# Optimization experiments

Measured on AMD Instinct MI355X. Metric: run time of the kernel, lower is better.

The kernel has to match this reference:

```python
import jax, jax.numpy as jnp
import numpy as np

B, IN_F, OUT_F = 1024, 256, 256
GRID_SIZE, K = 5, 3  # grid_size, spline_order
N_BASIS = GRID_SIZE + K


def _make_grid():
    h = (1.0 - (-1.0)) / GRID_SIZE
    return jnp.linspace(-1.0 - K * h, 1.0 + K * h, GRID_SIZE + 2 * K + 1, dtype=jnp.float32)


def compute_bspline_basis(x, grid, k):
    # x: (N,), grid: (G + 2k + 1,) -> (N, G + k)
    x = x[:, None]
    bases = ((x >= grid[:-1]) & (x < grid[1:])).astype(x.dtype)
    for p in range(1, k + 1):
        n = bases.shape[1] - 1
        left_den = jnp.clip(grid[p:p + n] - grid[:n], 1e-8)
        left = (x - grid[:n]) / left_den * bases[:, :n]
        right_den = jnp.clip(grid[p + 1:p + 1 + n] - grid[1:1 + n], 1e-8)
        right = (grid[p + 1:p + 1 + n] - x) / right_den * bases[:, 1:1 + n]
        bases = left + right
    # boundary fix: x at/above last interior knot falls into last basis
    bases = bases.at[:, -1].add((x[:, 0] >= grid[-k - 1]).astype(x.dtype))
    return bases


def setup_inputs() -> dict:
    key = jax.random.key(0)
    kx, kc, kb = jax.random.split(key, 3)
    x = jax.random.normal(kx, (B, IN_F), dtype=jnp.float32)
    coeff = jax.random.normal(kc, (OUT_F, IN_F, N_BASIS), dtype=jnp.float32) / np.sqrt(IN_F * N_BASIS)
    base_weight = jax.random.normal(kb, (OUT_F, IN_F), dtype=jnp.float32) / np.sqrt(IN_F)
    spline_weight = jnp.ones((OUT_F, IN_F), dtype=jnp.float32)
    grid = _make_grid()
    return {"x": x, "grid": grid, "coeff": coeff,
            "base_weight": base_weight, "spline_weight": spline_weight}


def reference(x, grid, coeff, base_weight, spline_weight):
    batch = x.shape[0]
    bases = compute_bspline_basis(x.reshape(-1), grid, K)          # (B*in, n_basis)
    bases = bases.reshape(batch, IN_F, N_BASIS)                     # (b, i, n)
    spline_out = jnp.einsum('bin,oin->boi', bases, coeff)           # (b, o, i)
    spline_out = spline_out * spline_weight[None, :, :]
    base_out = jax.nn.silu(x)[:, None, :] * base_weight[None, :, :]  # (b, o, i)
    return (spline_out + base_out).sum(axis=2)                      # (b, o)
```

## Files before the change

### kernel.cpp

```cpp
#include <hip/hip_runtime.h>
#include <hip/hip_bf16.h>

#define B_SZ   1024
#define IN_F   256
#define OUT_F  256
#define NB     9
#define KTOT   (IN_F * NB)
#define NGRID  12

typedef __attribute__((ext_vector_type(8))) short  bf16x8;
typedef __attribute__((ext_vector_type(16))) float f32x16;

__global__ __launch_bounds__(256) void kan_prep(
    const float* __restrict__ x,
    const float* __restrict__ grid,
    const float* __restrict__ coeff,
    const float* __restrict__ bw,
    const float* __restrict__ sw,
    __hip_bfloat16* __restrict__ phi,
    __hip_bfloat16* __restrict__ W) {
  if (blockIdx.x < (B_SZ * IN_F) / 256) {
    int idx = blockIdx.x * 256 + threadIdx.x;
    float g[NGRID];
#pragma unroll
    for (int j = 0; j < NGRID; ++j) g[j] = grid[j];
    float xv = x[idx];

    float bas[NGRID - 1];
#pragma unroll
    for (int j = 0; j < NGRID - 1; ++j)
      bas[j] = (xv >= g[j] && xv < g[j + 1]) ? 1.0f : 0.0f;

#pragma unroll
    for (int p = 1; p <= 3; ++p) {
      int n = NGRID - 1 - p;
#pragma unroll
      for (int j = 0; j < n; ++j) {
        float ld = g[p + j] - g[j];
        if (ld < 1e-8f) ld = 1e-8f;
        float rd = g[p + 1 + j] - g[j + 1];
        if (rd < 1e-8f) rd = 1e-8f;
        bas[j] = (xv - g[j]) * __builtin_amdgcn_rcpf(ld) * bas[j] +
                 (g[p + 1 + j] - xv) * __builtin_amdgcn_rcpf(rd) * bas[j + 1];
      }
    }
    bas[7] += (xv >= g[NGRID - 4]) ? 1.0f : 0.0f;
    float sil = xv / (1.0f + __expf(-xv));

    int b = idx >> 8;
    int i = idx & 255;
    __hip_bfloat16* dst = phi + b * KTOT + i;
#pragma unroll
    for (int n = 0; n < 8; ++n) dst[n * IN_F] = __float2bfloat16(bas[n]);
    dst[8 * IN_F] = __float2bfloat16(sil);
  } else {
    int idx = (blockIdx.x - (B_SZ * IN_F) / 256) * 256 + threadIdx.x;
    int o = idx >> 8;
    int i = idx & 255;
    float s = sw[idx];
    const float* c = coeff + (size_t)idx * 8;
    __hip_bfloat16* dst = W + o * KTOT + i;
#pragma unroll
    for (int n = 0; n < 8; ++n)
      dst[n * IN_F] = __float2bfloat16(s * c[n]);
    dst[8 * IN_F] = __float2bfloat16(bw[idx]);
  }
}

#define KSEG (KTOT / 8)

__global__ __launch_bounds__(512) void kan_gemm(
    const __hip_bfloat16* __restrict__ phi,
    const __hip_bfloat16* __restrict__ W,
    float* __restrict__ out) {
  __shared__ float partial[8][32 * 32];

  int tid  = threadIdx.x;
  int wave = tid >> 6;
  int lane = tid & 63;
  int bm = (blockIdx.x & 31) * 32;
  int bn = (blockIdx.x >> 5) * 32;
  int r = lane & 31;
  int h = lane >> 5;

  const short* ap = (const short*)(phi + (size_t)(bm + r) * KTOT) + wave * KSEG + h * 8;
  const short* bp = (const short*)(W   + (size_t)(bn + r) * KTOT) + wave * KSEG + h * 8;

  f32x16 acc;
#pragma unroll
  for (int g = 0; g < 16; ++g) acc[g] = 0.0f;

#pragma unroll 6
  for (int k = 0; k < KSEG; k += 16) {
    bf16x8 a = *(const bf16x8*)(ap + k);
    bf16x8 b = *(const bf16x8*)(bp + k);
    acc = __builtin_amdgcn_mfma_f32_32x32x16_bf16(a, b, acc, 0, 0, 0);
  }

  float* pw = &partial[wave][0];
#pragma unroll
  for (int g = 0; g < 16; ++g) {
    int row = (g & 3) + 8 * (g >> 2) + 4 * h;
    pw[row * 32 + r] = acc[g];
  }
  __syncthreads();

  int e0 = tid * 2;
  float s0 = 0.0f, s1 = 0.0f;
#pragma unroll
  for (int w = 0; w < 8; ++w) {
    s0 += partial[w][e0];
    s1 += partial[w][e0 + 1];
  }
  int row = e0 >> 5, col = e0 & 31;
  float2 v = make_float2(s0, s1);
  *(float2*)&out[(size_t)(bm + row) * OUT_F + bn + col] = v;
}

extern "C" void kernel_launch(void* const* d_in, const int* in_sizes, int n_in,
                              void* d_out, int out_size, void* d_ws, size_t ws_size,
                              hipStream_t stream) {
  const float* x     = (const float*)d_in[0];
  const float* grid  = (const float*)d_in[1];
  const float* coeff = (const float*)d_in[2];
  const float* bw    = (const float*)d_in[3];
  const float* sw    = (const float*)d_in[4];
  float* out = (float*)d_out;

  __hip_bfloat16* phi = (__hip_bfloat16*)d_ws;
  __hip_bfloat16* W   = phi + (size_t)B_SZ * KTOT;

  kan_prep<<<(B_SZ * IN_F + OUT_F * IN_F) / 256, 256, 0, stream>>>(
      x, grid, coeff, bw, sw, phi, W);
  kan_gemm<<<(B_SZ / 32) * (OUT_F / 32), 512, 0, stream>>>(phi, W, out);
}
```

Before: 76.75 us.

## Fuse prep and GEMM into one cooperative kernel with grid sync

Merges the basis/weight preparation kernel and the MFMA GEMM kernel into a single cooperative launch of 256 blocks of 512 threads. Each thread computes two activation rows' worth of basis values and possibly one weight entry, then a grid-wide barrier separates the prep and GEMM phases. This removes one kernel launch and the gap between them. The cost is a grid sync and a cooperative launch with fewer threads doing the prep work.

```diff
diff --git a/kernel.cpp b/kernel.cpp
--- a/kernel.cpp
+++ b/kernel.cpp
@@ -1,5 +1,8 @@
 #include <hip/hip_runtime.h>
 #include <hip/hip_bf16.h>
+#include <hip/hip_cooperative_groups.h>
+
+namespace cg = cooperative_groups;
 
 #define B_SZ   1024
 #define IN_F   256
@@ -7,73 +10,79 @@
 #define NB     9
 #define KTOT   (IN_F * NB)
 #define NGRID  12
+#define NTHR   (256 * 512)
 
 typedef __attribute__((ext_vector_type(8))) short  bf16x8;
 typedef __attribute__((ext_vector_type(16))) float f32x16;
 
-__global__ __launch_bounds__(256) void kan_prep(
+#define KSEG (KTOT / 8)
+
+__global__ __launch_bounds__(512) void kan_fused(
     const float* __restrict__ x,
     const float* __restrict__ grid,
     const float* __restrict__ coeff,
     const float* __restrict__ bw,
     const float* __restrict__ sw,
     __hip_bfloat16* __restrict__ phi,
-    __hip_bfloat16* __restrict__ W) {
-  if (blockIdx.x < (B_SZ * IN_F) / 256) {
-    int idx = blockIdx.x * 256 + threadIdx.x;
+    __hip_bfloat16* __restrict__ W,
+    float* __restrict__ out) {
+  __shared__ float partial[8][32 * 32];
+
+  int t = blockIdx.x * 512 + threadIdx.x;
+
+  {
     float g[NGRID];
 #pragma unroll
     for (int j = 0; j < NGRID; ++j) g[j] = grid[j];
-    float xv = x[idx];
-
-    float bas[NGRID - 1];
-#pragma unroll
-    for (int j = 0; j < NGRID - 1; ++j)
-      bas[j] = (xv >= g[j] && xv < g[j + 1]) ? 1.0f : 0.0f;
 
 #pragma unroll
-    for (int p = 1; p <= 3; ++p) {
-      int n = NGRID - 1 - p;
+    for (int rep = 0; rep < 2; ++rep) {
+      int idx = t + rep * NTHR;
+      float xv = x[idx];
+
+      float bas[NGRID - 1];
 #pragma unroll
-      for (int j = 0; j < n; ++j) {
-        float ld = g[p + j] - g[j];
-        if (ld < 1e-8f) ld = 1e-8f;
-        float rd = g[p + 1 + j] - g[j + 1];
-        if (rd < 1e-8f) rd = 1e-8f;
-        bas[j] = (xv - g[j]) * __builtin_amdgcn_rcpf(ld) * bas[j] +
-                 (g[p + 1 + j] - xv) * __builtin_amdgcn_rcpf(rd) * bas[j + 1];
+      for (int j = 0; j < NGRID - 1; ++j)
+        bas[j] = (xv >= g[j] && xv < g[j + 1]) ? 1.0f : 0.0f;
+
+#pragma unroll
+      for (int p = 1; p <= 3; ++p) {
+        int n = NGRID - 1 - p;
+#pragma unroll
+        for (int j = 0; j < n; ++j) {
+          float ld = g[p + j] - g[j];
+          if (ld < 1e-8f) ld = 1e-8f;
+          float rd = g[p + 1 + j] - g[j + 1];
+          if (rd < 1e-8f) rd = 1e-8f;
+          bas[j] = (xv - g[j]) * __builtin_amdgcn_rcpf(ld) * bas[j] +
+                   (g[p + 1 + j] - xv) * __builtin_amdgcn_rcpf(rd) * bas[j + 1];
+        }
       }
+      bas[7] += (xv >= g[NGRID - 4]) ? 1.0f : 0.0f;
+      float sil = xv / (1.0f + __expf(-xv));
+
+      int b = idx >> 8;
+      int i = idx & 255;
+      __hip_bfloat16* dst = phi + b * KTOT + i;
+#pragma unroll
+      for (int n = 0; n < 8; ++n) dst[n * IN_F] = __float2bfloat16(bas[n]);
+      dst[8 * IN_F] = __float2bfloat16(sil);
     }
-    bas[7] += (xv >= g[NGRID - 4]) ? 1.0f : 0.0f;
-    float sil = xv / (1.0f + __expf(-xv));
+  }
 
-    int b = idx >> 8;
-    int i = idx & 255;
-    __hip_bfloat16* dst = phi + b * KTOT + i;
-#pragma unroll
-    for (int n = 0; n < 8; ++n) dst[n * IN_F] = __float2bfloat16(bas[n]);
-    dst[8 * IN_F] = __float2bfloat16(sil);
-  } else {
-    int idx = (blockIdx.x - (B_SZ * IN_F) / 256) * 256 + threadIdx.x;
-    int o = idx >> 8;
-    int i = idx & 255;
-    float s = sw[idx];
-    const float* c = coeff + (size_t)idx * 8;
+  if (t < OUT_F * IN_F) {
+    int o = t >> 8;
+    int i = t & 255;
+    float s = sw[t];
+    const float* c = coeff + (size_t)t * 8;
     __hip_bfloat16* dst = W + o * KTOT + i;
 #pragma unroll
     for (int n = 0; n < 8; ++n)
       dst[n * IN_F] = __float2bfloat16(s * c[n]);
-    dst[8 * IN_F] = __float2bfloat16(bw[idx]);
+    dst[8 * IN_F] = __float2bfloat16(bw[t]);
   }
-}
 
-#define KSEG (KTOT / 8)
-
-__global__ __launch_bounds__(512) void kan_gemm(
-    const __hip_bfloat16* __restrict__ phi,
-    const __hip_bfloat16* __restrict__ W,
-    float* __restrict__ out) {
-  __shared__ float partial[8][32 * 32];
+  cg::this_grid().sync();
 
   int tid  = threadIdx.x;
   int wave = tid >> 6;
@@ -88,7 +97,7 @@
 
   f32x16 acc;
 #pragma unroll
-  for (int g = 0; g < 16; ++g) acc[g] = 0.0f;
+  for (int gg = 0; gg < 16; ++gg) acc[gg] = 0.0f;
 
 #pragma unroll 6
   for (int k = 0; k < KSEG; k += 16) {
@@ -99,9 +108,9 @@
 
   float* pw = &partial[wave][0];
 #pragma unroll
-  for (int g = 0; g < 16; ++g) {
-    int row = (g & 3) + 8 * (g >> 2) + 4 * h;
-    pw[row * 32 + r] = acc[g];
+  for (int gg = 0; gg < 16; ++gg) {
+    int row = (gg & 3) + 8 * (gg >> 2) + 4 * h;
+    pw[row * 32 + r] = acc[gg];
   }
   __syncthreads();
 
@@ -130,7 +139,7 @@
   __hip_bfloat16* phi = (__hip_bfloat16*)d_ws;
   __hip_bfloat16* W   = phi + (size_t)B_SZ * KTOT;
 
-  kan_prep<<<(B_SZ * IN_F + OUT_F * IN_F) / 256, 256, 0, stream>>>(
-      x, grid, coeff, bw, sw, phi, W);
-  kan_gemm<<<(B_SZ / 32) * (OUT_F / 32), 512, 0, stream>>>(phi, W, out);
+  void* args[] = {&x, &grid, &coeff, &bw, &sw, &phi, &W, &out};
+  hipLaunchCooperativeKernel((void*)kan_fused, dim3(256), dim3(512),
+                             args, 0, stream);
 }
```

Result: slower. 115.3 us (+50.2%).
